# Performance work log

Hardware: AMD Instinct MI355X
Metric: run time of the kernel (lower is better)

## Reference

```python
import jax, jax.numpy as jnp
import numpy as np

E = 20000      # num edges
S = 64         # mul of 0e (scalar) channels
V = 32         # mul of 1o (vector) channels
FC_IN = 128    # radial basis length
HID = 64       # fc hidden width
INV_SQRT3 = 0.5773502691896258  # CG(1o x 1o -> 0e) = delta_ij / sqrt(3)


def setup_inputs() -> dict:
    key = jax.random.key(0)
    ks = jax.random.split(key, 16)
    n = jax.random.normal
    return {
        # edge features, layout [64 scalars | 32 vectors * 3 comps]
        "fea_in1": n(ks[0], (E, S + 3 * V), jnp.float32),
        "fea_in2": n(ks[1], (E, S + 3 * V), jnp.float32),
        "fea_weight": n(ks[2], (E, FC_IN), jnp.float32),
        # FullyConnectedTensorProduct internal weights (e3nn init: normal(0,1))
        "w_ss_s": n(ks[3], (S, S, S), jnp.float32),   # 0e x 0e -> 64x0e scalars
        "w_vv_s": n(ks[4], (V, V, S), jnp.float32),   # 1o x 1o -> 64x0e scalars
        "w_ss_g": n(ks[5], (S, S, V), jnp.float32),   # 0e x 0e -> 32x0e gates
        "w_vv_g": n(ks[6], (V, V, V), jnp.float32),   # 1o x 1o -> 32x0e gates
        "w_sv_v": n(ks[7], (S, V, V), jnp.float32),   # 0e x 1o -> 32x1o
        "w_vs_v": n(ks[8], (V, S, V), jnp.float32),   # 1o x 0e -> 32x1o
        # fc MLP: Linear(128,64) SiLU Linear(64,64) SiLU Linear(64,96)
        "fc_w1": n(ks[9], (FC_IN, HID), jnp.float32) / np.sqrt(FC_IN).astype(np.float32),
        "fc_b1": jnp.zeros((HID,), jnp.float32),
        "fc_w2": n(ks[10], (HID, HID), jnp.float32) / np.sqrt(HID).astype(np.float32),
        "fc_b2": jnp.zeros((HID,), jnp.float32),
        "fc_w3": n(ks[11], (HID, S + V), jnp.float32) / np.sqrt(HID).astype(np.float32),
        "fc_b3": jnp.zeros((S + V,), jnp.float32),
        "batch_edge": jnp.zeros((E,), jnp.int32),  # unused (norm='')
    }


def _equiconv(fea_in1, fea_in2, fea_weight,
              w_ss_s, w_vv_s, w_ss_g, w_vv_g, w_sv_v, w_vs_v,
              fc_w1, fc_b1, fc_w2, fc_b2, fc_w3, fc_b3):
    x1s, x1v = fea_in1[:, :S], fea_in1[:, S:].reshape(-1, V, 3)
    x2s, x2v = fea_in2[:, :S], fea_in2[:, S:].reshape(-1, V, 3)

    # path normalization: 1/sqrt(fan_in), fan_in = sum(mul1*mul2) over paths to output
    a_sc = 1.0 / np.sqrt(S * S + V * V).astype(np.float32)
    a_vec = 1.0 / np.sqrt(2 * S * V).astype(np.float32)

    # FullyConnectedTensorProduct (uvw connectivity)
    sc = a_sc * (jnp.einsum('eu,ev,uvw->ew', x1s, x2s, w_ss_s)
                 + INV_SQRT3 * jnp.einsum('eui,evi,uvw->ew', x1v, x2v, w_vv_s))
    g = a_sc * (jnp.einsum('eu,ev,uvw->ew', x1s, x2s, w_ss_g)
                + INV_SQRT3 * jnp.einsum('eui,evi,uvw->ew', x1v, x2v, w_vv_g))
    vec = a_vec * (jnp.einsum('eu,evi,uvw->ewi', x1s, x2v, w_sv_v)
                   + jnp.einsum('eui,ev,uvw->ewi', x1v, x2s, w_vs_v))

    # Gate: silu on scalars, sigmoid gates multiply the l>0 part
    sc = jax.nn.silu(sc)
    vec = vec * jax.nn.sigmoid(g)[:, :, None]

    # fc MLP producing per-channel elementwise conv weights
    h = jax.nn.silu(fea_weight @ fc_w1 + fc_b1)
    h = jax.nn.silu(h @ fc_w2 + fc_b2)
    w = h @ fc_w3 + fc_b3  # [E, S+V]

    # e3ElementWise: one scalar weight per channel (shared over m components)
    sc = sc * w[:, :S]
    vec = vec * w[:, S:, None]
    return jnp.concatenate([sc, vec.reshape(-1, 3 * V)], axis=-1)


def reference(fea_in1, fea_in2, fea_weight,
              w_ss_s, w_vv_s, w_ss_g, w_vv_g, w_sv_v, w_vs_v,
              fc_w1, fc_b1, fc_w2, fc_b2, fc_w3, fc_b3, batch_edge):
    del batch_edge  # only used by optional e3LayerNorm (norm='')
    return _equiconv(fea_in1, fea_in2, fea_weight,
                     w_ss_s, w_vv_s, w_ss_g, w_vv_g, w_sv_v, w_vs_v,
                     fc_w1, fc_b1, fc_w2, fc_b2, fc_w3, fc_b3)
```

## Files before the change

kernel.cpp:

```cpp
#include <hip/hip_runtime.h>


#define E_TOT 20000

typedef __attribute__((ext_vector_type(8))) short short8;
typedef __attribute__((ext_vector_type(4))) float f32x4;
typedef __attribute__((ext_vector_type(2))) __bf16 bf16x2;

#define FRAG_USH 512
#define CH_USH   3072
#define N_CH     52
#define STRIDE_W 159744
#define FC1_OFF  638976
#define FC2_OFF  647168
#define FC3_OFF  651264
#define WS_USH   657408

__device__ __forceinline__ unsigned short f2b(float f){
  return __builtin_bit_cast(unsigned short, (__bf16)f);
}
__device__ __forceinline__ unsigned f2b2(float lo, float hi){
  bf16x2 t; t[0] = (__bf16)lo; t[1] = (__bf16)hi;
  return __builtin_bit_cast(unsigned, t);
}
__device__ __forceinline__ float b2f(unsigned short h){
  return __uint_as_float(((unsigned)h) << 16);
}
__device__ __forceinline__ f32x4 mfma16(short8 a, short8 b, f32x4 c){
  return __builtin_amdgcn_mfma_f32_16x16x32_bf16(a, b, c, 0, 0, 0);
}
union U8 { short8 v; unsigned u[4]; };
__device__ __forceinline__ float silu_f(float x){ return x/(1.f+__expf(-x)); }
__device__ __forceinline__ float sigm_f(float x){ return 1.f/(1.f+__expf(-x)); }

#define PACK8(a, s, x) \
  a.u[0]=f2b2((s)*(x)[0],(s)*(x)[1]); a.u[1]=f2b2((s)*(x)[2],(s)*(x)[3]); \
  a.u[2]=f2b2((s)*(x)[4],(s)*(x)[5]); a.u[3]=f2b2((s)*(x)[6],(s)*(x)[7]);

#define WAITV6 { __builtin_amdgcn_s_waitcnt(0xF76);  __builtin_amdgcn_sched_barrier(0); }
#define WAITV0 { __builtin_amdgcn_s_waitcnt(0xF70);  __builtin_amdgcn_sched_barrier(0); }
#define WAITL0 { __builtin_amdgcn_s_waitcnt(0xC07F); __builtin_amdgcn_sched_barrier(0); }

__device__ __forceinline__ int fpos(int kl, int n16){
  return (kl>>3)*128 + n16*8 + (kl&7);
}

__global__ void prep_weights(const float* __restrict__ ss_s, const float* __restrict__ ss_g,
                             const float* __restrict__ vv_s, const float* __restrict__ vv_g,
                             const float* __restrict__ sv,   const float* __restrict__ vs,
                             const float* __restrict__ w1,   const float* __restrict__ w2,
                             const float* __restrict__ w3,   unsigned short* __restrict__ wsb)
{
  int g = blockIdx.x * 256 + threadIdx.x;
  if (g >= WS_USH/8) return;
  const int dest = g << 3;
  const float A_SC  = 0.013975424859373686f;
  const float A_VV  = (float)(0.013975424859373686 * 0.5773502691896258);
  const float A_VEC = 0.015625f;

  const float* src = nullptr;
  int stride = 0;
  float scale = 1.f;

  if (dest < FC1_OFF) {
    int wave = dest / STRIDE_W;
    int off  = dest - wave*STRIDE_W;
    int c    = off / CH_USH;
    int rem  = off - c*CH_USH;
    int t    = rem >> 9;
    int p    = rem & 511;
    int kl   = (p >> 7) << 3;
    int n16  = (p >> 3) & 15;
    if (c < 32) {
      int u = (wave<<4) + (c>>1);
      int v = ((c&1)<<5) + kl;
      if (t < 4) { src = ss_s + (u<<12)+(v<<6)+((t<<4)+n16);     stride = 64; }
      else       { src = ss_g + (u<<11)+(v<<5)+(((t-4)<<4)+n16); stride = 32; }
      scale = A_SC;
    } else if (c < 40) {
      int u = (wave<<3) + (c-32);
      int v = kl;
      if (t < 4) { src = vv_s + (u<<11)+(v<<6)+((t<<4)+n16);     stride = 64; }
      else       { src = vv_g + (u<<10)+(v<<5)+(((t-4)<<4)+n16); stride = 32; }
      scale = A_VV;
    } else if (c < 46) {
      int ul = (c-40)*3 + (t>>1);
      if (ul < 16) {
        int u = (wave<<4) + ul;
        src = sv + (u<<10)+(kl<<5)+(((t&1)<<4)+n16);
        stride = 32; scale = A_VEC;
      }
    } else {
      int cc = c - 46;
      int vh = cc/3, ch3 = cc - vh*3;
      int fseq = ch3*6 + t;
      if (fseq < 16) {
        int u = (wave<<3) + (fseq>>1);
        int v = (vh<<5) + kl;
        src = vs + (u<<11)+(v<<5)+(((fseq&1)<<4)+n16);
        stride = 32; scale = A_VEC;
      }
    }
  } else if (dest < FC2_OFF) {
    int off = dest - FC1_OFF;
    int fi = off >> 9, p = off & 511;
    int kl = (p>>7)<<3, n16 = (p>>3)&15;
    int k = ((fi>>2)<<5) + kl, n = ((fi&3)<<4) + n16;
    src = w1 + (k<<6) + n; stride = 64;
  } else if (dest < FC3_OFF) {
    int off = dest - FC2_OFF;
    int fi = off >> 9, p = off & 511;
    int kl = (p>>7)<<3, n16 = (p>>3)&15;
    int k = ((fi>>2)<<5) + kl, n = ((fi&3)<<4) + n16;
    src = w2 + (k<<6) + n; stride = 64;
  } else {
    int off = dest - FC3_OFF;
    int fi = off >> 9, p = off & 511;
    int kl = (p>>7)<<3, n16 = (p>>3)&15;
    int koff = fi/6, nhi = fi - koff*6;
    int k = (koff<<5) + kl, n = (nhi<<4) + n16;
    src = w3 + k*96 + n; stride = 96;
  }

  U8 a;
  if (src) {
    float v0 = scale * src[0*stride], v1 = scale * src[1*stride];
    float v2 = scale * src[2*stride], v3 = scale * src[3*stride];
    float v4 = scale * src[4*stride], v5 = scale * src[5*stride];
    float v6 = scale * src[6*stride], v7 = scale * src[7*stride];
    a.u[0] = f2b2(v0, v1); a.u[1] = f2b2(v2, v3);
    a.u[2] = f2b2(v4, v5); a.u[3] = f2b2(v6, v7);
  } else {
    a.u[0] = 0; a.u[1] = 0; a.u[2] = 0; a.u[3] = 0;
  }
  *(short8*)(wsb + dest) = a.v;
}

__global__ __launch_bounds__(256, 2)
void equiconv_main(const float* __restrict__ fea1,
                   const float* __restrict__ fea2,
                   const float* __restrict__ few,
                   const float* __restrict__ fb1,
                   const float* __restrict__ fb2,
                   const float* __restrict__ fb3,
                   const unsigned short* __restrict__ wsb,
                   float* __restrict__ out)
{
  __shared__ __align__(16) unsigned short ring[4*2*CH_USH];
  __shared__ __align__(16) unsigned short x1s[32][66];
  __shared__ __align__(16) unsigned short x1v[32][98];
  __shared__ __align__(16) unsigned short hb[4][16][72];

  const int tid  = threadIdx.x;
  const int lane = tid & 63, wv = tid >> 6;
  const int ln   = lane & 15, quad = lane >> 4, q8 = quad << 3;
  const int ebase = blockIdx.x << 5;

  for (int it = tid; it < 1280; it += 256){
    int row = it / 40, seg = it - row*40;
    float4 v1 = *(const float4*)(fea1 + (size_t)(ebase + row)*160 + seg*4);
    const float* p1 = (const float*)&v1;
    int c0 = seg*4;
    #pragma unroll
    for (int jj = 0; jj < 4; jj++){
      int col = c0 + jj;
      if (col < 64) x1s[row][col] = f2b(p1[jj]);
      else          x1v[row][col-64] = f2b(p1[jj]);
    }
  }
  __syncthreads();

  float xe[2][8], xo[2][8], y0[2][8], y1[2][8], y2[2][8];
  #pragma unroll
  for (int s = 0; s < 2; s++){
    const float* p = fea2 + (size_t)(ebase + s*16 + ln)*160;
    float4 a0 = *(const float4*)(p + q8);
    float4 a1 = *(const float4*)(p + q8 + 4);
    float4 b0 = *(const float4*)(p + 32 + q8);
    float4 b1 = *(const float4*)(p + 36 + q8);
    xe[s][0]=a0.x; xe[s][1]=a0.y; xe[s][2]=a0.z; xe[s][3]=a0.w;
    xe[s][4]=a1.x; xe[s][5]=a1.y; xe[s][6]=a1.z; xe[s][7]=a1.w;
    xo[s][0]=b0.x; xo[s][1]=b0.y; xo[s][2]=b0.z; xo[s][3]=b0.w;
    xo[s][4]=b1.x; xo[s][5]=b1.y; xo[s][6]=b1.z; xo[s][7]=b1.w;
    const float* py = p + 64 + q8*3;
    float yb[24];
    #pragma unroll
    for (int t = 0; t < 12; t++){
      float2 f2v = *(const float2*)(py + 2*t);
      yb[2*t] = f2v.x; yb[2*t+1] = f2v.y;
    }
    #pragma unroll
    for (int j = 0; j < 8; j++){
      y0[s][j] = yb[3*j]; y1[s][j] = yb[3*j+1]; y2[s][j] = yb[3*j+2];
    }
  }

  const unsigned short* gstream = wsb + (size_t)wv*STRIDE_W;
  const int rbase = wv*2*CH_USH;
  auto issue_chunk = [&](int c){
    const unsigned short* g = gstream + c*CH_USH + lane*8;
    unsigned short* l = &ring[rbase + (c&1)*CH_USH];
    #pragma unroll
    for (int q = 0; q < 6; q++)
      __builtin_amdgcn_global_load_lds(
        (const __attribute__((address_space(1))) unsigned int*)(g + q*FRAG_USH),
        (__attribute__((address_space(3))) unsigned int*)(l + q*FRAG_USH),
        16, 0, 0);
  };
  issue_chunk(0); issue_chunk(1);

  const int r0 = ln, r1 = 16 + ln;
  const f32x4 z4 = {0.f,0.f,0.f,0.f};
  f32x4 accS[2][6] = {{z4,z4,z4,z4,z4,z4},{z4,z4,z4,z4,z4,z4}};
  f32x4 accV[2][3][2] = {{{z4,z4},{z4,z4},{z4,z4}},{{z4,z4},{z4,z4},{z4,z4}}};

  #define READ6(c, bb) { \
    const unsigned short* sl = &ring[rbase + ((c)&1)*CH_USH + lane*8]; \
    _Pragma("unroll") for (int t = 0; t < 6; t++) bb[t] = *(const short8*)(sl + t*FRAG_USH); }
  #define STEP(c) { WAITL0; if ((c)+2 < N_CH) issue_chunk((c)+2); }

  #pragma unroll 2
  for (int c = 0; c < 32; c++){
    int u = (wv<<4) + (c>>1);
    float s0 = b2f(x1s[r0][u]);
    float s1 = b2f(x1s[r1][u]);
    WAITV6;
    short8 bb[6]; READ6(c, bb); STEP(c);
    U8 a0, a1;
    if (c & 1){ PACK8(a0, s0, xo[0]); PACK8(a1, s1, xo[1]); }
    else      { PACK8(a0, s0, xe[0]); PACK8(a1, s1, xe[1]); }
    #pragma unroll
    for (int t = 0; t < 6; t++){
      accS[0][t] = mfma16(a0.v, bb[t], accS[0][t]);
      accS[1][t] = mfma16(a1.v, bb[t], accS[1][t]);
    }
  }
  #pragma unroll 1
  for (int k8 = 0; k8 < 8; k8++){
    int c = 32 + k8, u = (wv<<3) + k8;
    U8 a[2];
    #pragma unroll
    for (int s = 0; s < 2; s++){
      int rr = s ? r1 : r0;
      float c0 = b2f(x1v[rr][u*3+0]);
      float c1 = b2f(x1v[rr][u*3+1]);
      float c2 = b2f(x1v[rr][u*3+2]);
      float pv[8];
      #pragma unroll
      for (int j = 0; j < 8; j++)
        pv[j] = c0*y0[s][j] + c1*y1[s][j] + c2*y2[s][j];
      a[s].u[0]=f2b2(pv[0],pv[1]); a[s].u[1]=f2b2(pv[2],pv[3]);
      a[s].u[2]=f2b2(pv[4],pv[5]); a[s].u[3]=f2b2(pv[6],pv[7]);
    }
    WAITV6;
    short8 bb[6]; READ6(c, bb); STEP(c);
    #pragma unroll
    for (int t = 0; t < 6; t++){
      accS[0][t] = mfma16(a[0].v, bb[t], accS[0][t]);
      accS[1][t] = mfma16(a[1].v, bb[t], accS[1][t]);
    }
  }
  #pragma unroll 1
  for (int ch = 0; ch < 6; ch++){
    int c = 40 + ch;
    WAITV6;
    short8 bb[6]; READ6(c, bb); STEP(c);
    #pragma unroll
    for (int uu = 0; uu < 3; uu++){
      int ui = ch*3 + uu;
      if (ui < 16){
        int u = (wv<<4) + ui;
        float s0 = b2f(x1s[r0][u]);
        float s1 = b2f(x1s[r1][u]);
        U8 a[2][3];
        PACK8(a[0][0], s0, y0[0]); PACK8(a[0][1], s0, y1[0]); PACK8(a[0][2], s0, y2[0]);
        PACK8(a[1][0], s1, y0[1]); PACK8(a[1][1], s1, y1[1]); PACK8(a[1][2], s1, y2[1]);
        #pragma unroll
        for (int t = 0; t < 2; t++){
          short8 b8 = bb[uu*2 + t];
          #pragma unroll
          for (int s = 0; s < 2; s++)
            #pragma unroll
            for (int i = 0; i < 3; i++)
              accV[s][i][t] = mfma16(a[s][i].v, b8, accV[s][i][t]);
        }
      }
    }
  }
  #pragma unroll 1
  for (int pc = 0; pc < 6; pc++){
    int p = pc / 3, ch = pc - p*3;
    int c = 46 + pc;
    if (pc < 5) { WAITV6 }
    else        { WAITV0 }
    short8 bb[6]; READ6(c, bb); STEP(c);
    #pragma unroll
    for (int uu = 0; uu < 3; uu++){
      int ui = ch*3 + uu;
      if (ui < 8){
        int u = (wv<<3) + ui;
        U8 a[2][3];
        #pragma unroll
        for (int s = 0; s < 2; s++){
          int rr = s ? r1 : r0;
          float c0 = b2f(x1v[rr][u*3+0]);
          float c1 = b2f(x1v[rr][u*3+1]);
          float c2 = b2f(x1v[rr][u*3+2]);
          const float* xx = p ? xo[s] : xe[s];
          PACK8(a[s][0], c0, xx); PACK8(a[s][1], c1, xx); PACK8(a[s][2], c2, xx);
        }
        #pragma unroll
        for (int t = 0; t < 2; t++){
          short8 b8 = bb[uu*2 + t];
          #pragma unroll
          for (int s = 0; s < 2; s++)
            #pragma unroll
            for (int i = 0; i < 3; i++)
              accV[s][i][t] = mfma16(a[s][i].v, b8, accV[s][i][t]);
        }
      }
    }
  }

  f32x4 T0[12], T1[12];
  #pragma unroll
  for (int t = 0; t < 6; t++){ T0[t] = accS[0][t]; T1[t] = accS[1][t]; }
  #pragma unroll
  for (int t = 0; t < 2; t++)
    #pragma unroll
    for (int i = 0; i < 3; i++){
      T0[6+3*t+i] = accV[0][i][t]; T1[6+3*t+i] = accV[1][i][t];
    }

  float* redf = (float*)ring;
  #define PUT12(base, T) { _Pragma("unroll") for (int j=0;j<12;j++) \
    *(f32x4*)(redf + ((base)+j)*320 + ln*20 + (quad<<2)) = T[j]; }
  #define ADD12(base, T) { _Pragma("unroll") for (int j=0;j<12;j++) \
    T[j] += *(const f32x4*)(redf + ((base)+j)*320 + ln*20 + (quad<<2)); }

  __syncthreads();
  if (wv==1) PUT12(0, T0);  if (wv==2) PUT12(12, T1);
  __syncthreads();
  if (wv==0) ADD12(0, T0);  if (wv==3) ADD12(12, T1);
  __syncthreads();
  if (wv==2) PUT12(0, T0);  if (wv==1) PUT12(12, T1);
  __syncthreads();
  if (wv==0) ADD12(0, T0);  if (wv==3) ADD12(12, T1);
  __syncthreads();
  if (wv==3) PUT12(0, T0);  if (wv==0) PUT12(12, T1);
  __syncthreads();
  if (wv==0) ADD12(0, T0);  if (wv==3) ADD12(12, T1);

  if (wv == 1 || wv == 2) return;
  const int s = (wv == 0) ? 0 : 1;
  f32x4* P = (wv == 0) ? T0 : T1;

  f32x4 accF[4] = {z4,z4,z4,z4};
  {
    const float* fwp = few + (size_t)(ebase + s*16 + ln)*128;
    const short8* B = (const short8*)(wsb + FC1_OFF);
    #pragma unroll
    for (int c = 0; c < 4; c++){
      float4 fa  = *(const float4*)(fwp + c*32 + q8);
      float4 fbv = *(const float4*)(fwp + c*32 + q8 + 4);
      U8 a;
      a.u[0]=f2b2(fa.x,fa.y);   a.u[1]=f2b2(fa.z,fa.w);
      a.u[2]=f2b2(fbv.x,fbv.y); a.u[3]=f2b2(fbv.z,fbv.w);
      #pragma unroll
      for (int t = 0; t < 4; t++) accF[t] = mfma16(a.v, B[(c*4+t)*64 + lane], accF[t]);
    }
  }
  #pragma unroll
  for (int t = 0; t < 4; t++){
    float bb = fb1[(t<<4)+ln];
    #pragma unroll
    for (int r = 0; r < 4; r++)
      hb[wv][(quad<<2)+r][(t<<4)+ln] = f2b(silu_f(accF[t][r] + bb));
  }
  f32x4 acc2[4] = {z4,z4,z4,z4};
  {
    const short8* B = (const short8*)(wsb + FC2_OFF);
    #pragma unroll
    for (int c = 0; c < 2; c++){
      uint4 hq = *(const uint4*)&hb[wv][ln][c*32 + q8];
      U8 a; a.u[0]=hq.x; a.u[1]=hq.y; a.u[2]=hq.z; a.u[3]=hq.w;
      #pragma unroll
      for (int t = 0; t < 4; t++) acc2[t] = mfma16(a.v, B[(c*4+t)*64 + lane], acc2[t]);
    }
  }
  #pragma unroll
  for (int t = 0; t < 4; t++){
    float bb = fb2[(t<<4)+ln];
    #pragma unroll
    for (int r = 0; r < 4; r++)
      hb[wv][(quad<<2)+r][(t<<4)+ln] = f2b(silu_f(acc2[t][r] + bb));
  }
  f32x4 acc3[6] = {z4,z4,z4,z4,z4,z4};
  {
    const short8* B = (const short8*)(wsb + FC3_OFF);
    #pragma unroll
    for (int c = 0; c < 2; c++){
      uint4 hq = *(const uint4*)&hb[wv][ln][c*32 + q8];
      U8 a; a.u[0]=hq.x; a.u[1]=hq.y; a.u[2]=hq.z; a.u[3]=hq.w;
      #pragma unroll
      for (int t = 0; t < 6; t++) acc3[t] = mfma16(a.v, B[(c*6+t)*64 + lane], acc3[t]);
    }
  }

  #pragma unroll
  for (int r = 0; r < 4; r++){
    int eg = ebase + s*16 + (quad<<2) + r;
    float* op = out + (size_t)eg*160;
    #pragma unroll
    for (int t = 0; t < 4; t++)
      op[(t<<4)+ln] = silu_f(P[t][r]) * (acc3[t][r] + fb3[(t<<4)+ln]);
    #pragma unroll
    for (int tp = 0; tp < 2; tp++){
      int wc = (tp<<4) + ln;
      float f = sigm_f(P[4+tp][r]) * (acc3[4+tp][r] + fb3[64+wc]);
      op[64 + wc*3 + 0] = P[6+3*tp+0][r] * f;
      op[64 + wc*3 + 1] = P[6+3*tp+1][r] * f;
      op[64 + wc*3 + 2] = P[6+3*tp+2][r] * f;
    }
  }
}

extern "C" void kernel_launch(void* const* d_in, const int* in_sizes, int n_in,
                              void* d_out, int out_size, void* d_ws, size_t ws_size,
                              hipStream_t stream) {
  (void)in_sizes; (void)n_in; (void)out_size; (void)ws_size;
  unsigned short* wsb = (unsigned short*)d_ws;

  prep_weights<<<(WS_USH/8 + 255)/256, 256, 0, stream>>>(
      (const float*)d_in[3], (const float*)d_in[5],
      (const float*)d_in[4], (const float*)d_in[6],
      (const float*)d_in[7], (const float*)d_in[8],
      (const float*)d_in[9], (const float*)d_in[11], (const float*)d_in[13],
      wsb);

  equiconv_main<<<E_TOT/32, 256, 0, stream>>>(
      (const float*)d_in[0], (const float*)d_in[1], (const float*)d_in[2],
      (const float*)d_in[10], (const float*)d_in[12], (const float*)d_in[14],
      (const unsigned short*)wsb, (float*)d_out);
}
```

Measured before the change: 178.8 us.

## Deepen weight streaming ring to 11 half-chunk slots with 10 in flight

Replaces the double-buffered per-wave chunk ring with an 11-slot ring of half-chunks, keeping up to 10 global-to-LDS loads in flight and waiting with explicit vmcnt codes per half-chunk. The vector-path loops are re-sliced so each half-chunk's three fragments are consumed as soon as they land, with a hand-unrolled tail that drains the queue using decreasing wait counts. LDS grows to about 145 KB in one pooled buffer that is reused for the reduction and hidden activations, and launch bounds drop to one block per CU. The aim is to hide the latency of streaming weights from global memory, at the cost of lower occupancy and fragile hand-tuned wait counts.

New measurement: 218.0 us. +21.9%, slower.

```diff
diff --git a/kernel.cpp b/kernel.cpp
--- a/kernel.cpp
+++ b/kernel.cpp
@@ -8,14 +8,22 @@
 typedef __attribute__((ext_vector_type(2))) __bf16 bf16x2;
 
 #define FRAG_USH 512
+#define HALF_USH 1536
 #define CH_USH   3072
 #define N_CH     52
+#define NH       104
+#define NSLOT    11
 #define STRIDE_W 159744
 #define FC1_OFF  638976
 #define FC2_OFF  647168
 #define FC3_OFF  651264
 #define WS_USH   657408
 
+#define RING_B   135168
+#define X1S_OFF  135168
+#define X1V_OFF  139392
+#define POOL_B   145664
+
 __device__ __forceinline__ unsigned short f2b(float f){
   return __builtin_bit_cast(unsigned short, (__bf16)f);
 }
@@ -37,9 +45,7 @@
   a.u[0]=f2b2((s)*(x)[0],(s)*(x)[1]); a.u[1]=f2b2((s)*(x)[2],(s)*(x)[3]); \
   a.u[2]=f2b2((s)*(x)[4],(s)*(x)[5]); a.u[3]=f2b2((s)*(x)[6],(s)*(x)[7]);
 
-#define WAITV6 { __builtin_amdgcn_s_waitcnt(0xF76);  __builtin_amdgcn_sched_barrier(0); }
-#define WAITV0 { __builtin_amdgcn_s_waitcnt(0xF70);  __builtin_amdgcn_sched_barrier(0); }
-#define WAITL0 { __builtin_amdgcn_s_waitcnt(0xC07F); __builtin_amdgcn_sched_barrier(0); }
+#define WV(code) { __builtin_amdgcn_s_waitcnt(code); __builtin_amdgcn_sched_barrier(0); }
 
 __device__ __forceinline__ int fpos(int kl, int n16){
   return (kl>>3)*128 + n16*8 + (kl&7);
@@ -136,7 +142,7 @@
   *(short8*)(wsb + dest) = a.v;
 }
 
-__global__ __launch_bounds__(256, 2)
+__global__ __launch_bounds__(256, 1)
 void equiconv_main(const float* __restrict__ fea1,
                    const float* __restrict__ fea2,
                    const float* __restrict__ few,
@@ -146,10 +152,16 @@
                    const unsigned short* __restrict__ wsb,
                    float* __restrict__ out)
 {
-  __shared__ __align__(16) unsigned short ring[4*2*CH_USH];
-  __shared__ __align__(16) unsigned short x1s[32][66];
-  __shared__ __align__(16) unsigned short x1v[32][98];
-  __shared__ __align__(16) unsigned short hb[4][16][72];
+  __shared__ __align__(16) unsigned char pool[POOL_B];
+  unsigned short* ring = (unsigned short*)pool;
+  unsigned short* x1s_ = (unsigned short*)(pool + X1S_OFF);
+  unsigned short* x1v_ = (unsigned short*)(pool + X1V_OFF);
+  unsigned short* hb_  = (unsigned short*)(pool + X1S_OFF);
+  float*          redf = (float*)pool;
+
+  #define X1S(r, cc) x1s_[(r)*66 + (cc)]
+  #define X1V(r, cc) x1v_[(r)*98 + (cc)]
+  #define HB(w, r, cc) hb_[(((w)<<4) + (r))*72 + (cc)]
 
   const int tid  = threadIdx.x;
   const int lane = tid & 63, wv = tid >> 6;
@@ -164,8 +176,8 @@
     #pragma unroll
     for (int jj = 0; jj < 4; jj++){
       int col = c0 + jj;
-      if (col < 64) x1s[row][col] = f2b(p1[jj]);
-      else          x1v[row][col-64] = f2b(p1[jj]);
+      if (col < 64) X1S(row, col) = f2b(p1[jj]);
+      else          X1V(row, col-64) = f2b(p1[jj]);
     }
   }
   __syncthreads();
@@ -196,43 +208,53 @@
   }
 
   const unsigned short* gstream = wsb + (size_t)wv*STRIDE_W;
-  const int rbase = wv*2*CH_USH;
-  auto issue_chunk = [&](int c){
-    const unsigned short* g = gstream + c*CH_USH + lane*8;
-    unsigned short* l = &ring[rbase + (c&1)*CH_USH];
-    #pragma unroll
-    for (int q = 0; q < 6; q++)
+  const int rbase = wv*NSLOT*HALF_USH;
+  auto issue_half = [&](int h){
+    const unsigned short* g = gstream + h*HALF_USH + lane*8;
+    unsigned short* l = &ring[rbase + (h%NSLOT)*HALF_USH];
+    #pragma unroll
+    for (int q = 0; q < 3; q++)
       __builtin_amdgcn_global_load_lds(
         (const __attribute__((address_space(1))) unsigned int*)(g + q*FRAG_USH),
         (__attribute__((address_space(3))) unsigned int*)(l + q*FRAG_USH),
         16, 0, 0);
   };
-  issue_chunk(0); issue_chunk(1);
+  #pragma unroll
+  for (int h = 0; h < 10; h++) issue_half(h);
 
   const int r0 = ln, r1 = 16 + ln;
   const f32x4 z4 = {0.f,0.f,0.f,0.f};
   f32x4 accS[2][6] = {{z4,z4,z4,z4,z4,z4},{z4,z4,z4,z4,z4,z4}};
   f32x4 accV[2][3][2] = {{{z4,z4},{z4,z4},{z4,z4}},{{z4,z4},{z4,z4},{z4,z4}}};
 
-  #define READ6(c, bb) { \
-    const unsigned short* sl = &ring[rbase + ((c)&1)*CH_USH + lane*8]; \
-    _Pragma("unroll") for (int t = 0; t < 6; t++) bb[t] = *(const short8*)(sl + t*FRAG_USH); }
-  #define STEP(c) { WAITL0; if ((c)+2 < N_CH) issue_chunk((c)+2); }
+  #define RSTEP(hh, bb, WCODE, DOISS) { \
+    const int h_ = (hh); \
+    WV(WCODE); \
+    { const unsigned short* sl_ = &ring[rbase + (h_%NSLOT)*HALF_USH + lane*8]; \
+      _Pragma("unroll") for (int t_ = 0; t_ < 3; t_++) bb[t_] = *(const short8*)(sl_ + t_*FRAG_USH); } \
+    __builtin_amdgcn_sched_barrier(0); \
+    if (DOISS) issue_half(h_ + 10); }
 
   #pragma unroll 2
   for (int c = 0; c < 32; c++){
     int u = (wv<<4) + (c>>1);
-    float s0 = b2f(x1s[r0][u]);
-    float s1 = b2f(x1s[r1][u]);
-    WAITV6;
-    short8 bb[6]; READ6(c, bb); STEP(c);
+    float s0 = b2f(X1S(r0, u));
+    float s1 = b2f(X1S(r1, u));
     U8 a0, a1;
     if (c & 1){ PACK8(a0, s0, xo[0]); PACK8(a1, s1, xo[1]); }
     else      { PACK8(a0, s0, xe[0]); PACK8(a1, s1, xe[1]); }
-    #pragma unroll
-    for (int t = 0; t < 6; t++){
+    short8 bb[3];
+    RSTEP(2*c, bb, 0x4F7B, 1);
+    #pragma unroll
+    for (int t = 0; t < 3; t++){
       accS[0][t] = mfma16(a0.v, bb[t], accS[0][t]);
       accS[1][t] = mfma16(a1.v, bb[t], accS[1][t]);
+    }
+    RSTEP(2*c+1, bb, 0x4F7B, 1);
+    #pragma unroll
+    for (int t = 0; t < 3; t++){
+      accS[0][3+t] = mfma16(a0.v, bb[t], accS[0][3+t]);
+      accS[1][3+t] = mfma16(a1.v, bb[t], accS[1][3+t]);
     }
   }
   #pragma unroll 1
@@ -242,9 +264,9 @@
     #pragma unroll
     for (int s = 0; s < 2; s++){
       int rr = s ? r1 : r0;
-      float c0 = b2f(x1v[rr][u*3+0]);
-      float c1 = b2f(x1v[rr][u*3+1]);
-      float c2 = b2f(x1v[rr][u*3+2]);
+      float c0 = b2f(X1V(rr, u*3+0));
+      float c1 = b2f(X1V(rr, u*3+1));
+      float c2 = b2f(X1V(rr, u*3+2));
       float pv[8];
       #pragma unroll
       for (int j = 0; j < 8; j++)
@@ -252,75 +274,126 @@
       a[s].u[0]=f2b2(pv[0],pv[1]); a[s].u[1]=f2b2(pv[2],pv[3]);
       a[s].u[2]=f2b2(pv[4],pv[5]); a[s].u[3]=f2b2(pv[6],pv[7]);
     }
-    WAITV6;
-    short8 bb[6]; READ6(c, bb); STEP(c);
-    #pragma unroll
-    for (int t = 0; t < 6; t++){
+    short8 bb[3];
+    RSTEP(2*c, bb, 0x4F7B, 1);
+    #pragma unroll
+    for (int t = 0; t < 3; t++){
       accS[0][t] = mfma16(a[0].v, bb[t], accS[0][t]);
       accS[1][t] = mfma16(a[1].v, bb[t], accS[1][t]);
+    }
+    RSTEP(2*c+1, bb, 0x4F7B, 1);
+    #pragma unroll
+    for (int t = 0; t < 3; t++){
+      accS[0][3+t] = mfma16(a[0].v, bb[t], accS[0][3+t]);
+      accS[1][3+t] = mfma16(a[1].v, bb[t], accS[1][3+t]);
     }
   }
   #pragma unroll 1
   for (int ch = 0; ch < 6; ch++){
     int c = 40 + ch;
-    WAITV6;
-    short8 bb[6]; READ6(c, bb); STEP(c);
-    #pragma unroll
-    for (int uu = 0; uu < 3; uu++){
-      int ui = ch*3 + uu;
-      if (ui < 16){
-        int u = (wv<<4) + ui;
-        float s0 = b2f(x1s[r0][u]);
-        float s1 = b2f(x1s[r1][u]);
-        U8 a[2][3];
-        PACK8(a[0][0], s0, y0[0]); PACK8(a[0][1], s0, y1[0]); PACK8(a[0][2], s0, y2[0]);
-        PACK8(a[1][0], s1, y0[1]); PACK8(a[1][1], s1, y1[1]); PACK8(a[1][2], s1, y2[1]);
+    int u0 = (wv<<4) + ch*3;
+    short8 bb[3];
+    RSTEP(2*c, bb, 0x4F7B, 1);
+    {
+      float s0 = b2f(X1S(r0, u0)), s1 = b2f(X1S(r1, u0));
+      U8 a[2][3];
+      PACK8(a[0][0], s0, y0[0]); PACK8(a[0][1], s0, y1[0]); PACK8(a[0][2], s0, y2[0]);
+      PACK8(a[1][0], s1, y0[1]); PACK8(a[1][1], s1, y1[1]); PACK8(a[1][2], s1, y2[1]);
+      #pragma unroll
+      for (int s = 0; s < 2; s++)
         #pragma unroll
-        for (int t = 0; t < 2; t++){
-          short8 b8 = bb[uu*2 + t];
+        for (int i = 0; i < 3; i++){
+          accV[s][i][0] = mfma16(a[s][i].v, bb[0], accV[s][i][0]);
+          accV[s][i][1] = mfma16(a[s][i].v, bb[1], accV[s][i][1]);
+        }
+      if (ch < 5){
+        float t0v = b2f(X1S(r0, u0+1)), t1v = b2f(X1S(r1, u0+1));
+        U8 b[2][3];
+        PACK8(b[0][0], t0v, y0[0]); PACK8(b[0][1], t0v, y1[0]); PACK8(b[0][2], t0v, y2[0]);
+        PACK8(b[1][0], t1v, y0[1]); PACK8(b[1][1], t1v, y1[1]); PACK8(b[1][2], t1v, y2[1]);
+        #pragma unroll
+        for (int s = 0; s < 2; s++)
           #pragma unroll
-          for (int s = 0; s < 2; s++)
-            #pragma unroll
-            for (int i = 0; i < 3; i++)
-              accV[s][i][t] = mfma16(a[s][i].v, b8, accV[s][i][t]);
+          for (int i = 0; i < 3; i++)
+            accV[s][i][0] = mfma16(b[s][i].v, bb[2], accV[s][i][0]);
+      }
+    }
+    RSTEP(2*c+1, bb, 0x4F7B, 1);
+    if (ch < 5){
+      float t0v = b2f(X1S(r0, u0+1)), t1v = b2f(X1S(r1, u0+1));
+      U8 b[2][3];
+      PACK8(b[0][0], t0v, y0[0]); PACK8(b[0][1], t0v, y1[0]); PACK8(b[0][2], t0v, y2[0]);
+      PACK8(b[1][0], t1v, y0[1]); PACK8(b[1][1], t1v, y1[1]); PACK8(b[1][2], t1v, y2[1]);
+      #pragma unroll
+      for (int s = 0; s < 2; s++)
+        #pragma unroll
+        for (int i = 0; i < 3; i++)
+          accV[s][i][1] = mfma16(b[s][i].v, bb[0], accV[s][i][1]);
+      float v0 = b2f(X1S(r0, u0+2)), v1s = b2f(X1S(r1, u0+2));
+      U8 d[2][3];
+      PACK8(d[0][0], v0, y0[0]);  PACK8(d[0][1], v0, y1[0]);  PACK8(d[0][2], v0, y2[0]);
+      PACK8(d[1][0], v1s, y0[1]); PACK8(d[1][1], v1s, y1[1]); PACK8(d[1][2], v1s, y2[1]);
+      #pragma unroll
+      for (int s = 0; s < 2; s++)
+        #pragma unroll
+        for (int i = 0; i < 3; i++){
+          accV[s][i][0] = mfma16(d[s][i].v, bb[1], accV[s][i][0]);
+          accV[s][i][1] = mfma16(d[s][i].v, bb[2], accV[s][i][1]);
         }
-      }
-    }
-  }
-  #pragma unroll 1
-  for (int pc = 0; pc < 6; pc++){
-    int p = pc / 3, ch = pc - p*3;
-    int c = 46 + pc;
-    if (pc < 5) { WAITV6 }
-    else        { WAITV0 }
-    short8 bb[6]; READ6(c, bb); STEP(c);
-    #pragma unroll
-    for (int uu = 0; uu < 3; uu++){
-      int ui = ch*3 + uu;
-      if (ui < 8){
-        int u = (wv<<3) + ui;
-        U8 a[2][3];
-        #pragma unroll
-        for (int s = 0; s < 2; s++){
-          int rr = s ? r1 : r0;
-          float c0 = b2f(x1v[rr][u*3+0]);
-          float c1 = b2f(x1v[rr][u*3+1]);
-          float c2 = b2f(x1v[rr][u*3+2]);
-          const float* xx = p ? xo[s] : xe[s];
-          PACK8(a[s][0], c0, xx); PACK8(a[s][1], c1, xx); PACK8(a[s][2], c2, xx);
-        }
-        #pragma unroll
-        for (int t = 0; t < 2; t++){
-          short8 b8 = bb[uu*2 + t];
-          #pragma unroll
-          for (int s = 0; s < 2; s++)
-            #pragma unroll
-            for (int i = 0; i < 3; i++)
-              accV[s][i][t] = mfma16(a[s][i].v, b8, accV[s][i][t]);
-        }
-      }
-    }
-  }
+    }
+  }
+  #define VSPC(pcv, W0, DI0, W1, DI1) { \
+    const int p_ = (pcv)/3, ch_ = (pcv)%3, c_ = 46+(pcv); \
+    const int u0_ = (wv<<3) + ch_*3; \
+    short8 bb[3]; \
+    RSTEP(2*c_, bb, W0, DI0); \
+    { U8 a_[2][3]; \
+      _Pragma("unroll") for (int s_ = 0; s_ < 2; s_++){ \
+        int rr_ = s_ ? r1 : r0; \
+        float c0_ = b2f(X1V(rr_, u0_*3+0)), c1_ = b2f(X1V(rr_, u0_*3+1)), c2_ = b2f(X1V(rr_, u0_*3+2)); \
+        const float* xx_ = p_ ? xo[s_] : xe[s_]; \
+        PACK8(a_[s_][0], c0_, xx_); PACK8(a_[s_][1], c1_, xx_); PACK8(a_[s_][2], c2_, xx_); } \
+      _Pragma("unroll") for (int s_ = 0; s_ < 2; s_++) \
+        _Pragma("unroll") for (int i_ = 0; i_ < 3; i_++){ \
+          accV[s_][i_][0] = mfma16(a_[s_][i_].v, bb[0], accV[s_][i_][0]); \
+          accV[s_][i_][1] = mfma16(a_[s_][i_].v, bb[1], accV[s_][i_][1]); } \
+      U8 b_[2][3]; \
+      _Pragma("unroll") for (int s_ = 0; s_ < 2; s_++){ \
+        int rr_ = s_ ? r1 : r0; \
+        float c0_ = b2f(X1V(rr_, (u0_+1)*3+0)), c1_ = b2f(X1V(rr_, (u0_+1)*3+1)), c2_ = b2f(X1V(rr_, (u0_+1)*3+2)); \
+        const float* xx_ = p_ ? xo[s_] : xe[s_]; \
+        PACK8(b_[s_][0], c0_, xx_); PACK8(b_[s_][1], c1_, xx_); PACK8(b_[s_][2], c2_, xx_); } \
+      _Pragma("unroll") for (int s_ = 0; s_ < 2; s_++) \
+        _Pragma("unroll") for (int i_ = 0; i_ < 3; i_++) \
+          accV[s_][i_][0] = mfma16(b_[s_][i_].v, bb[2], accV[s_][i_][0]); } \
+    RSTEP(2*c_+1, bb, W1, DI1); \
+    { U8 b_[2][3]; \
+      _Pragma("unroll") for (int s_ = 0; s_ < 2; s_++){ \
+        int rr_ = s_ ? r1 : r0; \
+        float c0_ = b2f(X1V(rr_, (u0_+1)*3+0)), c1_ = b2f(X1V(rr_, (u0_+1)*3+1)), c2_ = b2f(X1V(rr_, (u0_+1)*3+2)); \
+        const float* xx_ = p_ ? xo[s_] : xe[s_]; \
+        PACK8(b_[s_][0], c0_, xx_); PACK8(b_[s_][1], c1_, xx_); PACK8(b_[s_][2], c2_, xx_); } \
+      _Pragma("unroll") for (int s_ = 0; s_ < 2; s_++) \
+        _Pragma("unroll") for (int i_ = 0; i_ < 3; i_++) \
+          accV[s_][i_][1] = mfma16(b_[s_][i_].v, bb[0], accV[s_][i_][1]); \
+      if (ch_ < 2){ \
+        U8 d_[2][3]; \
+        _Pragma("unroll") for (int s_ = 0; s_ < 2; s_++){ \
+          int rr_ = s_ ? r1 : r0; \
+          float c0_ = b2f(X1V(rr_, (u0_+2)*3+0)), c1_ = b2f(X1V(rr_, (u0_+2)*3+1)), c2_ = b2f(X1V(rr_, (u0_+2)*3+2)); \
+          const float* xx_ = p_ ? xo[s_] : xe[s_]; \
+          PACK8(d_[s_][0], c0_, xx_); PACK8(d_[s_][1], c1_, xx_); PACK8(d_[s_][2], c2_, xx_); } \
+        _Pragma("unroll") for (int s_ = 0; s_ < 2; s_++) \
+          _Pragma("unroll") for (int i_ = 0; i_ < 3; i_++){ \
+            accV[s_][i_][0] = mfma16(d_[s_][i_].v, bb[1], accV[s_][i_][0]); \
+            accV[s_][i_][1] = mfma16(d_[s_][i_].v, bb[2], accV[s_][i_][1]); } } } }
+
+  VSPC(0, 0x4F7B, 1, 0x4F7B, 1);
+  VSPC(1, 0x4F7B, 0, 0x4F78, 0);
+  VSPC(2, 0x4F75, 0, 0x4F72, 0);
+  VSPC(3, 0x0F7F, 0, 0x0F7C, 0);
+  VSPC(4, 0x0F79, 0, 0x0F76, 0);
+  VSPC(5, 0x0F73, 0, 0x0F70, 0);
 
   f32x4 T0[12], T1[12];
   #pragma unroll
@@ -332,7 +405,6 @@
       T0[6+3*t+i] = accV[0][i][t]; T1[6+3*t+i] = accV[1][i][t];
     }
 
-  float* redf = (float*)ring;
   #define PUT12(base, T) { _Pragma("unroll") for (int j=0;j<12;j++) \
     *(f32x4*)(redf + ((base)+j)*320 + ln*20 + (quad<<2)) = T[j]; }
   #define ADD12(base, T) { _Pragma("unroll") for (int j=0;j<12;j++) \
@@ -375,14 +447,14 @@
     float bb = fb1[(t<<4)+ln];
     #pragma unroll
     for (int r = 0; r < 4; r++)
-      hb[wv][(quad<<2)+r][(t<<4)+ln] = f2b(silu_f(accF[t][r] + bb));
+      HB(wv, (quad<<2)+r, (t<<4)+ln) = f2b(silu_f(accF[t][r] + bb));
   }
   f32x4 acc2[4] = {z4,z4,z4,z4};
   {
     const short8* B = (const short8*)(wsb + FC2_OFF);
     #pragma unroll
     for (int c = 0; c < 2; c++){
-      uint4 hq = *(const uint4*)&hb[wv][ln][c*32 + q8];
+      uint4 hq = *(const uint4*)&HB(wv, ln, c*32 + q8);
       U8 a; a.u[0]=hq.x; a.u[1]=hq.y; a.u[2]=hq.z; a.u[3]=hq.w;
       #pragma unroll
       for (int t = 0; t < 4; t++) acc2[t] = mfma16(a.v, B[(c*4+t)*64 + lane], acc2[t]);
@@ -393,14 +465,14 @@
     float bb = fb2[(t<<4)+ln];
     #pragma unroll
     for (int r = 0; r < 4; r++)
-      hb[wv][(quad<<2)+r][(t<<4)+ln] = f2b(silu_f(acc2[t][r] + bb));
+      HB(wv, (quad<<2)+r, (t<<4)+ln) = f2b(silu_f(acc2[t][r] + bb));
   }
   f32x4 acc3[6] = {z4,z4,z4,z4,z4,z4};
   {
     const short8* B = (const short8*)(wsb + FC3_OFF);
     #pragma unroll
     for (int c = 0; c < 2; c++){
-      uint4 hq = *(const uint4*)&hb[wv][ln][c*32 + q8];
+      uint4 hq = *(const uint4*)&HB(wv, ln, c*32 + q8);
       U8 a; a.u[0]=hq.x; a.u[1]=hq.y; a.u[2]=hq.z; a.u[3]=hq.w;
       #pragma unroll
       for (int t = 0; t < 6; t++) acc3[t] = mfma16(a.v, B[(c*6+t)*64 + lane], acc3[t]);
```

## Deepen weight-streaming pipeline to five half-chunk LDS slots with finer waits

Applied to the files above, without the earlier changes.

Replaces the per-wave double-buffered weight ring of full chunks with a five-slot ring of half-chunks, prefetching four halves ahead and waiting per half with vmcnt-based waits. The hb scratch buffer is aliased onto the x1s region in a single shared pool, keeping the LDS footprint about the same as before. The intent is more global-to-LDS loads in flight so MFMA work hides weight fetch latency. The cost is more complex waitcnt bookkeeping and a possible aliasing hazard, since hb reuses x1s after the main loop.

New measurement: 176.1 us. Within noise of the previous version (-1.5%).

```diff
diff --git a/kernel.cpp b/kernel.cpp
--- a/kernel.cpp
+++ b/kernel.cpp
@@ -8,14 +8,20 @@
 typedef __attribute__((ext_vector_type(2))) __bf16 bf16x2;
 
 #define FRAG_USH 512
+#define HALF_USH 1536
 #define CH_USH   3072
 #define N_CH     52
+#define NSLOT    5
 #define STRIDE_W 159744
 #define FC1_OFF  638976
 #define FC2_OFF  647168
 #define FC3_OFF  651264
 #define WS_USH   657408
 
+#define X1S_OFF  61440
+#define X1V_OFF  65664
+#define POOL_B   71936
+
 __device__ __forceinline__ unsigned short f2b(float f){
   return __builtin_bit_cast(unsigned short, (__bf16)f);
 }
@@ -37,9 +43,8 @@
   a.u[0]=f2b2((s)*(x)[0],(s)*(x)[1]); a.u[1]=f2b2((s)*(x)[2],(s)*(x)[3]); \
   a.u[2]=f2b2((s)*(x)[4],(s)*(x)[5]); a.u[3]=f2b2((s)*(x)[6],(s)*(x)[7]);
 
-#define WAITV6 { __builtin_amdgcn_s_waitcnt(0xF76);  __builtin_amdgcn_sched_barrier(0); }
-#define WAITV0 { __builtin_amdgcn_s_waitcnt(0xF70);  __builtin_amdgcn_sched_barrier(0); }
-#define WAITL0 { __builtin_amdgcn_s_waitcnt(0xC07F); __builtin_amdgcn_sched_barrier(0); }
+#define WV(code) { __builtin_amdgcn_s_waitcnt(code); __builtin_amdgcn_sched_barrier(0); }
+#define WL3      { __builtin_amdgcn_s_waitcnt(0xC37F); __builtin_amdgcn_sched_barrier(0); }
 
 __device__ __forceinline__ int fpos(int kl, int n16){
   return (kl>>3)*128 + n16*8 + (kl&7);
@@ -146,10 +151,16 @@
                    const unsigned short* __restrict__ wsb,
                    float* __restrict__ out)
 {
-  __shared__ __align__(16) unsigned short ring[4*2*CH_USH];
-  __shared__ __align__(16) unsigned short x1s[32][66];
-  __shared__ __align__(16) unsigned short x1v[32][98];
-  __shared__ __align__(16) unsigned short hb[4][16][72];
+  __shared__ __align__(16) unsigned char pool[POOL_B];
+  unsigned short* ring = (unsigned short*)pool;
+  unsigned short* x1s_ = (unsigned short*)(pool + X1S_OFF);
+  unsigned short* x1v_ = (unsigned short*)(pool + X1V_OFF);
+  unsigned short* hb_  = (unsigned short*)(pool + X1S_OFF);
+  float*          redf = (float*)pool;
+
+  #define X1S(r, cc) x1s_[(r)*66 + (cc)]
+  #define X1V(r, cc) x1v_[(r)*98 + (cc)]
+  #define HB(w, r, cc) hb_[(((w)<<4) + (r))*72 + (cc)]
 
   const int tid  = threadIdx.x;
   const int lane = tid & 63, wv = tid >> 6;
@@ -164,8 +175,8 @@
     #pragma unroll
     for (int jj = 0; jj < 4; jj++){
       int col = c0 + jj;
-      if (col < 64) x1s[row][col] = f2b(p1[jj]);
-      else          x1v[row][col-64] = f2b(p1[jj]);
+      if (col < 64) X1S(row, col) = f2b(p1[jj]);
+      else          X1V(row, col-64) = f2b(p1[jj]);
     }
   }
   __syncthreads();
@@ -196,39 +207,52 @@
   }
 
   const unsigned short* gstream = wsb + (size_t)wv*STRIDE_W;
-  const int rbase = wv*2*CH_USH;
-  auto issue_chunk = [&](int c){
-    const unsigned short* g = gstream + c*CH_USH + lane*8;
-    unsigned short* l = &ring[rbase + (c&1)*CH_USH];
-    #pragma unroll
-    for (int q = 0; q < 6; q++)
+  const int rbase = wv*NSLOT*HALF_USH;
+  auto issue_half = [&](int h){
+    const unsigned short* g = gstream + h*HALF_USH + lane*8;
+    unsigned short* l = &ring[rbase + (h%NSLOT)*HALF_USH];
+    #pragma unroll
+    for (int q = 0; q < 3; q++)
       __builtin_amdgcn_global_load_lds(
         (const __attribute__((address_space(1))) unsigned int*)(g + q*FRAG_USH),
         (__attribute__((address_space(3))) unsigned int*)(l + q*FRAG_USH),
         16, 0, 0);
   };
-  issue_chunk(0); issue_chunk(1);
+  issue_half(0); issue_half(1); issue_half(2); issue_half(3);
 
   const int r0 = ln, r1 = 16 + ln;
   const f32x4 z4 = {0.f,0.f,0.f,0.f};
   f32x4 accS[2][6] = {{z4,z4,z4,z4,z4,z4},{z4,z4,z4,z4,z4,z4}};
   f32x4 accV[2][3][2] = {{{z4,z4},{z4,z4},{z4,z4}},{{z4,z4},{z4,z4},{z4,z4}}};
 
-  #define READ6(c, bb) { \
-    const unsigned short* sl = &ring[rbase + ((c)&1)*CH_USH + lane*8]; \
-    _Pragma("unroll") for (int t = 0; t < 6; t++) bb[t] = *(const short8*)(sl + t*FRAG_USH); }
-  #define STEP(c) { WAITL0; if ((c)+2 < N_CH) issue_chunk((c)+2); }
+  #define READCH(cc, bb, WAC, WBC, DOISS) { \
+    const int h0_ = 2*(cc); \
+    const int sA_ = h0_ % NSLOT, sB_ = (h0_+1) % NSLOT; \
+    WV(WAC); \
+    { const unsigned short* pA_ = &ring[rbase + sA_*HALF_USH + lane*8]; \
+      bb[0] = *(const short8*)(pA_); \
+      bb[1] = *(const short8*)(pA_ + FRAG_USH); \
+      bb[2] = *(const short8*)(pA_ + 2*FRAG_USH); } \
+    __builtin_amdgcn_sched_barrier(0); \
+    if (DOISS) issue_half(h0_ + 4); \
+    WV(WBC); \
+    { const unsigned short* pB_ = &ring[rbase + sB_*HALF_USH + lane*8]; \
+      bb[3] = *(const short8*)(pB_); \
+      bb[4] = *(const short8*)(pB_ + FRAG_USH); \
+      bb[5] = *(const short8*)(pB_ + 2*FRAG_USH); } \
+    __builtin_amdgcn_sched_barrier(0); \
+    if (DOISS) { WL3; issue_half(h0_ + 5); } }
 
   #pragma unroll 2
   for (int c = 0; c < 32; c++){
     int u = (wv<<4) + (c>>1);
-    float s0 = b2f(x1s[r0][u]);
-    float s1 = b2f(x1s[r1][u]);
-    WAITV6;
-    short8 bb[6]; READ6(c, bb); STEP(c);
+    float s0 = b2f(X1S(r0, u));
+    float s1 = b2f(X1S(r1, u));
     U8 a0, a1;
     if (c & 1){ PACK8(a0, s0, xo[0]); PACK8(a1, s1, xo[1]); }
     else      { PACK8(a0, s0, xe[0]); PACK8(a1, s1, xe[1]); }
+    short8 bb[6];
+    READCH(c, bb, 0x0F79, 0x0F79, 1);
     #pragma unroll
     for (int t = 0; t < 6; t++){
       accS[0][t] = mfma16(a0.v, bb[t], accS[0][t]);
@@ -242,9 +266,9 @@
     #pragma unroll
     for (int s = 0; s < 2; s++){
       int rr = s ? r1 : r0;
-      float c0 = b2f(x1v[rr][u*3+0]);
-      float c1 = b2f(x1v[rr][u*3+1]);
-      float c2 = b2f(x1v[rr][u*3+2]);
+      float c0 = b2f(X1V(rr, u*3+0));
+      float c1 = b2f(X1V(rr, u*3+1));
+      float c2 = b2f(X1V(rr, u*3+2));
       float pv[8];
       #pragma unroll
       for (int j = 0; j < 8; j++)
@@ -252,8 +276,8 @@
       a[s].u[0]=f2b2(pv[0],pv[1]); a[s].u[1]=f2b2(pv[2],pv[3]);
       a[s].u[2]=f2b2(pv[4],pv[5]); a[s].u[3]=f2b2(pv[6],pv[7]);
     }
-    WAITV6;
-    short8 bb[6]; READ6(c, bb); STEP(c);
+    short8 bb[6];
+    READCH(c, bb, 0x0F79, 0x0F79, 1);
     #pragma unroll
     for (int t = 0; t < 6; t++){
       accS[0][t] = mfma16(a[0].v, bb[t], accS[0][t]);
@@ -263,15 +287,15 @@
   #pragma unroll 1
   for (int ch = 0; ch < 6; ch++){
     int c = 40 + ch;
-    WAITV6;
-    short8 bb[6]; READ6(c, bb); STEP(c);
+    short8 bb[6];
+    READCH(c, bb, 0x0F79, 0x0F79, 1);
     #pragma unroll
     for (int uu = 0; uu < 3; uu++){
       int ui = ch*3 + uu;
       if (ui < 16){
         int u = (wv<<4) + ui;
-        float s0 = b2f(x1s[r0][u]);
-        float s1 = b2f(x1s[r1][u]);
+        float s0 = b2f(X1S(r0, u));
+        float s1 = b2f(X1S(r1, u));
         U8 a[2][3];
         PACK8(a[0][0], s0, y0[0]); PACK8(a[0][1], s0, y1[0]); PACK8(a[0][2], s0, y2[0]);
         PACK8(a[1][0], s1, y0[1]); PACK8(a[1][1], s1, y1[1]); PACK8(a[1][2], s1, y2[1]);
@@ -287,39 +311,50 @@
       }
     }
   }
+  #define VSBODY(pcv, bb) { \
+    const int p_ = (pcv)/3, ch_ = (pcv) - p_*3; \
+    _Pragma("unroll") \
+    for (int uu = 0; uu < 3; uu++){ \
+      int ui = ch_*3 + uu; \
+      if (ui < 8){ \
+        int u = (wv<<3) + ui; \
+        U8 a[2][3]; \
+        _Pragma("unroll") \
+        for (int s = 0; s < 2; s++){ \
+          int rr = s ? r1 : r0; \
+          float c0 = b2f(X1V(rr, u*3+0)); \
+          float c1 = b2f(X1V(rr, u*3+1)); \
+          float c2 = b2f(X1V(rr, u*3+2)); \
+          const float* xx = p_ ? xo[s] : xe[s]; \
+          PACK8(a[s][0], c0, xx); PACK8(a[s][1], c1, xx); PACK8(a[s][2], c2, xx); \
+        } \
+        _Pragma("unroll") \
+        for (int t = 0; t < 2; t++){ \
+          short8 b8 = bb[uu*2 + t]; \
+          _Pragma("unroll") \
+          for (int s = 0; s < 2; s++) \
+            _Pragma("unroll") \
+            for (int i = 0; i < 3; i++) \
+              accV[s][i][t] = mfma16(a[s][i].v, b8, accV[s][i][t]); \
+        } \
+      } \
+    } }
+
   #pragma unroll 1
-  for (int pc = 0; pc < 6; pc++){
-    int p = pc / 3, ch = pc - p*3;
-    int c = 46 + pc;
-    if (pc < 5) { WAITV6 }
-    else        { WAITV0 }
-    short8 bb[6]; READ6(c, bb); STEP(c);
-    #pragma unroll
-    for (int uu = 0; uu < 3; uu++){
-      int ui = ch*3 + uu;
-      if (ui < 8){
-        int u = (wv<<3) + ui;
-        U8 a[2][3];
-        #pragma unroll
-        for (int s = 0; s < 2; s++){
-          int rr = s ? r1 : r0;
-          float c0 = b2f(x1v[rr][u*3+0]);
-          float c1 = b2f(x1v[rr][u*3+1]);
-          float c2 = b2f(x1v[rr][u*3+2]);
-          const float* xx = p ? xo[s] : xe[s];
-          PACK8(a[s][0], c0, xx); PACK8(a[s][1], c1, xx); PACK8(a[s][2], c2, xx);
-        }
-        #pragma unroll
-        for (int t = 0; t < 2; t++){
-          short8 b8 = bb[uu*2 + t];
-          #pragma unroll
-          for (int s = 0; s < 2; s++)
-            #pragma unroll
-            for (int i = 0; i < 3; i++)
-              accV[s][i][t] = mfma16(a[s][i].v, b8, accV[s][i][t]);
-        }
-      }
-    }
+  for (int pc = 0; pc < 4; pc++){
+    short8 bb[6];
+    READCH(46+pc, bb, 0x0F79, 0x0F79, 1);
+    VSBODY(pc, bb);
+  }
+  {
+    short8 bb[6];
+    READCH(50, bb, 0x0F79, 0x0F76, 0);
+    VSBODY(4, bb);
+  }
+  {
+    short8 bb[6];
+    READCH(51, bb, 0x0F73, 0x0F70, 0);
+    VSBODY(5, bb);
   }
 
   f32x4 T0[12], T1[12];
@@ -332,7 +367,6 @@
       T0[6+3*t+i] = accV[0][i][t]; T1[6+3*t+i] = accV[1][i][t];
     }
 
-  float* redf = (float*)ring;
   #define PUT12(base, T) { _Pragma("unroll") for (int j=0;j<12;j++) \
     *(f32x4*)(redf + ((base)+j)*320 + ln*20 + (quad<<2)) = T[j]; }
   #define ADD12(base, T) { _Pragma("unroll") for (int j=0;j<12;j++) \
@@ -375,14 +409,14 @@
     float bb = fb1[(t<<4)+ln];
     #pragma unroll
     for (int r = 0; r < 4; r++)
-      hb[wv][(quad<<2)+r][(t<<4)+ln] = f2b(silu_f(accF[t][r] + bb));
+      HB(wv, (quad<<2)+r, (t<<4)+ln) = f2b(silu_f(accF[t][r] + bb));
   }
   f32x4 acc2[4] = {z4,z4,z4,z4};
   {
     const short8* B = (const short8*)(wsb + FC2_OFF);
     #pragma unroll
     for (int c = 0; c < 2; c++){
-      uint4 hq = *(const uint4*)&hb[wv][ln][c*32 + q8];
+      uint4 hq = *(const uint4*)&HB(wv, ln, c*32 + q8);
       U8 a; a.u[0]=hq.x; a.u[1]=hq.y; a.u[2]=hq.z; a.u[3]=hq.w;
       #pragma unroll
       for (int t = 0; t < 4; t++) acc2[t] = mfma16(a.v, B[(c*4+t)*64 + lane], acc2[t]);
@@ -393,14 +427,14 @@
     float bb = fb2[(t<<4)+ln];
     #pragma unroll
     for (int r = 0; r < 4; r++)
-      hb[wv][(quad<<2)+r][(t<<4)+ln] = f2b(silu_f(acc2[t][r] + bb));
+      HB(wv, (quad<<2)+r, (t<<4)+ln) = f2b(silu_f(acc2[t][r] + bb));
   }
   f32x4 acc3[6] = {z4,z4,z4,z4,z4,z4};
   {
     const short8* B = (const short8*)(wsb + FC3_OFF);
     #pragma unroll
     for (int c = 0; c < 2; c++){
-      uint4 hq = *(const uint4*)&hb[wv][ln][c*32 + q8];
+      uint4 hq = *(const uint4*)&HB(wv, ln, c*32 + q8);
       U8 a; a.u[0]=hq.x; a.u[1]=hq.y; a.u[2]=hq.z; a.u[3]=hq.w;
       #pragma unroll
       for (int t = 0; t < 6; t++) acc3[t] = mfma16(a.v, B[(c*6+t)*64 + lane], acc3[t]);
```
